# Kernel optimization log

Hardware: AMD Instinct MI355X
Metric: run time of the kernel (lower is better)

The kernel has to match this reference:

```python
import jax, jax.numpy as jnp
import numpy as np
import math

N_EMBD = 768
N_HEAD = 8
HEAD_DIM = N_EMBD // N_HEAD


def new_gelu(x):
    c = math.sqrt(2.0 / math.pi)
    return 0.5 * x * (1.0 + jnp.tanh(c * (x + 0.044715 * x * x * x)))


def layer_norm(x, gamma, beta, eps=1e-5):
    mean = jnp.mean(x, axis=-1, keepdims=True)
    var = jnp.maximum(jnp.mean(x * x, axis=-1, keepdims=True) - mean * mean, 0.0)
    return (x - mean) * jax.lax.rsqrt(var + eps) * gamma + beta


def setup_inputs() -> dict:
    key = jax.random.key(0)
    ks = jax.random.split(key, 10)
    C = N_EMBD
    s = lambda n: 1.0 / math.sqrt(n)
    return {
        "x": jax.random.normal(ks[0], (8, 1024, C), dtype=jnp.float32),
        "ln1_g": jnp.ones((C,), jnp.float32),
        "ln1_b": jnp.zeros((C,), jnp.float32),
        "ln2_g": jnp.ones((C,), jnp.float32),
        "ln2_b": jnp.zeros((C,), jnp.float32),
        "W_attn": jax.random.normal(ks[1], (3 * C, C), jnp.float32) * s(C),
        "b_attn": jnp.zeros((3 * C,), jnp.float32),
        "W_proj": jax.random.normal(ks[2], (C, C), jnp.float32) * s(C),
        "b_proj": jnp.zeros((C,), jnp.float32),
        "W_fc": jax.random.normal(ks[3], (4 * C, C), jnp.float32) * s(C),
        "b_fc": jnp.zeros((4 * C,), jnp.float32),
        "W_fc_proj": jax.random.normal(ks[4], (C, 4 * C), jnp.float32) * s(4 * C),
        "b_fc_proj": jnp.zeros((C,), jnp.float32),
    }


def reference(x, ln1_g, ln1_b, ln2_g, ln2_b, W_attn, b_attn, W_proj, b_proj,
              W_fc, b_fc, W_fc_proj, b_fc_proj):
    B, T, C = x.shape
    # --- attention branch ---
    x1 = layer_norm(x, ln1_g, ln1_b)
    qkv = jnp.einsum('btc,oc->bto', x1, W_attn) + b_attn  # [B,T,3C]
    q, k, v = jnp.split(qkv, 3, axis=-1)
    q = q.reshape(B, T, N_HEAD, HEAD_DIM).transpose(0, 2, 1, 3)  # [B,H,T,D]
    k = k.reshape(B, T, N_HEAD, HEAD_DIM).transpose(0, 2, 1, 3)
    v = v.reshape(B, T, N_HEAD, HEAD_DIM).transpose(0, 2, 1, 3)
    att = jnp.einsum('bhqd,bhkd->bhqk', q, k) * (1.0 / math.sqrt(HEAD_DIM))
    causal = jnp.tril(jnp.ones((T, T), bool))
    att = jnp.where(causal[None, None], att, -jnp.inf)
    att = jax.nn.softmax(att, axis=-1)
    y = jnp.einsum('bhqk,bhkd->bhqd', att, v)
    y = y.transpose(0, 2, 1, 3).reshape(B, T, C)
    y = jnp.einsum('btc,oc->bto', y, W_proj) + b_proj
    x = x + y
    # --- MLP branch ---
    x2 = layer_norm(x, ln2_g, ln2_b)
    h = new_gelu(jnp.einsum('btc,oc->bto', x2, W_fc) + b_fc)
    m = jnp.einsum('bth,oh->bto', h, W_fc_proj) + b_fc_proj
    return x + m
```

## Files before the change

### kernel.cpp

```cpp
#include <hip/hip_runtime.h>
#include <math.h>


#define MROWS 8192
#define CDIM  768
#define TSEQ  1024

typedef _Float16 f16x8 __attribute__((ext_vector_type(8)));
typedef _Float16 f16x4 __attribute__((ext_vector_type(4)));
typedef float f32x4 __attribute__((ext_vector_type(4)));

__device__ __forceinline__ void async_copy16(void* lds, const void* g) {
    __builtin_amdgcn_global_load_lds(
        (const __attribute__((address_space(1))) unsigned int*)g,
        (__attribute__((address_space(3))) unsigned int*)lds, 16, 0, 0);
}

__device__ __forceinline__ int xcd_swizzle(int orig, int nwg) {
    int q = nwg >> 3, r = nwg & 7;
    int xcd = orig & 7, lid = orig >> 3;
    return (xcd < r ? xcd * (q + 1) : r * (q + 1) + (xcd - r) * q) + lid;
}

__device__ __forceinline__ float fast_gelu(float u) {
    float inner = 0.7978845608028654f * (u + 0.044715f * u * u * u);
    float e = __expf(2.0f * inner);
    float th = 1.0f - 2.0f / (e + 1.0f);
    return 0.5f * u * (1.0f + th);
}

__global__ __launch_bounds__(256) void f2h4_kernel(const float* __restrict__ i0,
                                                   const float* __restrict__ i1,
                                                   const float* __restrict__ i2,
                                                   const float* __restrict__ i3,
                                                   _Float16* __restrict__ o0,
                                                   _Float16* __restrict__ o1,
                                                   _Float16* __restrict__ o2,
                                                   _Float16* __restrict__ o3) {
    int bb = blockIdx.x;
    const float* in;
    _Float16* out;
    int lb;
    if (bb < 432)       { in = i0; out = o0; lb = bb; }
    else if (bb < 576)  { in = i1; out = o1; lb = bb - 432; }
    else if (bb < 1152) { in = i2; out = o2; lb = bb - 576; }
    else                { in = i3; out = o3; lb = bb - 1152; }
    int i = lb * 1024 + threadIdx.x;
#pragma unroll
    for (int p = 0; p < 4; ++p, i += 256) {
        float4 v = reinterpret_cast<const float4*>(in)[i];
        f16x4 h;
        h[0] = (_Float16)v.x; h[1] = (_Float16)v.y;
        h[2] = (_Float16)v.z; h[3] = (_Float16)v.w;
        reinterpret_cast<f16x4*>(out)[i] = h;
    }
}

__global__ __launch_bounds__(256) void ln_kernel(const float* __restrict__ x,
                                                 const float* __restrict__ g,
                                                 const float* __restrict__ bta,
                                                 _Float16* __restrict__ out) {
    int row = blockIdx.x;
    int t = threadIdx.x;
    const float* xr = x + (size_t)row * CDIM;
    float v0 = xr[t], v1 = xr[t + 256], v2 = xr[t + 512];
    float s = v0 + v1 + v2;
    float q = v0 * v0 + v1 * v1 + v2 * v2;
#pragma unroll
    for (int o = 32; o; o >>= 1) {
        s += __shfl_xor(s, o);
        q += __shfl_xor(q, o);
    }
    __shared__ float ls[4], lq[4];
    int w = t >> 6, lane = t & 63;
    if (lane == 0) { ls[w] = s; lq[w] = q; }
    __syncthreads();
    s = ls[0] + ls[1] + ls[2] + ls[3];
    q = lq[0] + lq[1] + lq[2] + lq[3];
    float mean = s * (1.0f / CDIM);
    float var = fmaxf(q * (1.0f / CDIM) - mean * mean, 0.0f);
    float rstd = rsqrtf(var + 1e-5f);
    _Float16* orow = out + (size_t)row * CDIM;
    orow[t]       = (_Float16)((v0 - mean) * rstd * g[t]       + bta[t]);
    orow[t + 256] = (_Float16)((v1 - mean) * rstd * g[t + 256] + bta[t + 256]);
    orow[t + 512] = (_Float16)((v2 - mean) * rstd * g[t + 512] + bta[t + 512]);
}

template <int EPI, typename OutT>
__global__ __launch_bounds__(256) void hgemm(const _Float16* __restrict__ A,
                                             const _Float16* __restrict__ W,
                                             const float* __restrict__ bias,
                                             const float* __restrict__ res,
                                             OutT* __restrict__ out,
                                             int M, int N, int K) {
    __shared__ _Float16 As[128 * 32];
    __shared__ _Float16 Bs[128 * 32];
    const int t = threadIdx.x;
    const int wid = t >> 6;
    const int l = t & 63;
    const int fr = l & 15;
    const int fq = l >> 4;
    const int wr = wid >> 1, wc = wid & 1;

    const int nx = gridDim.x;
    const int wg = xcd_swizzle(blockIdx.y * nx + blockIdx.x, nx * gridDim.y);
    const int row0 = (wg / nx) * 128, col0 = (wg % nx) * 128;

    const _Float16* ga = A + (size_t)row0 * K;
    const _Float16* gb = W + (size_t)col0 * K;

    f32x4 acc[4][4] = {};
    const int r_st = t >> 2, c_st = (t & 3) * 8;

    for (int k0 = 0; k0 < K; k0 += 32) {
        __syncthreads();
#pragma unroll
        for (int p = 0; p < 2; ++p) {
            char* la = (char*)As + wid * 1024 + p * 4096;
            char* lb = (char*)Bs + wid * 1024 + p * 4096;
            int r = r_st + p * 64;
            async_copy16(la, ga + (size_t)r * K + k0 + c_st);
            async_copy16(lb, gb + (size_t)r * K + k0 + c_st);
        }
        __syncthreads();

        f16x8 af[4], bf[4];
#pragma unroll
        for (int m = 0; m < 4; ++m)
            af[m] = *reinterpret_cast<const f16x8*>(&As[(wr * 64 + m * 16 + fr) * 32 + fq * 8]);
#pragma unroll
        for (int n = 0; n < 4; ++n)
            bf[n] = *reinterpret_cast<const f16x8*>(&Bs[(wc * 64 + n * 16 + fr) * 32 + fq * 8]);
#pragma unroll
        for (int m = 0; m < 4; ++m)
#pragma unroll
            for (int n = 0; n < 4; ++n)
                acc[m][n] = __builtin_amdgcn_mfma_f32_16x16x32_f16(af[m], bf[n], acc[m][n], 0, 0, 0);
    }

#pragma unroll
    for (int m = 0; m < 4; ++m) {
#pragma unroll
        for (int j = 0; j < 4; ++j) {
            int r = row0 + wr * 64 + m * 16 + fq * 4 + j;
#pragma unroll
            for (int n = 0; n < 4; ++n) {
                int c = col0 + wc * 64 + n * 16 + fr;
                float v = acc[m][n][j] + bias[c];
                if (EPI == 1) v += res[(size_t)r * N + c];
                if (EPI == 2) v = fast_gelu(v);
                out[(size_t)r * N + c] = (OutT)v;
            }
        }
    }
}

template <int EPI, typename OutT>
__global__ __launch_bounds__(256) void hgemm64(const _Float16* __restrict__ A,
                                               const _Float16* __restrict__ W,
                                               const float* __restrict__ bias,
                                               const float* __restrict__ res,
                                               OutT* __restrict__ out,
                                               int M, int N, int K) {
    __shared__ _Float16 As[64 * 32];
    __shared__ _Float16 Bs[128 * 32];
    const int t = threadIdx.x;
    const int wid = t >> 6;
    const int l = t & 63;
    const int fr = l & 15;
    const int fq = l >> 4;
    const int wr = wid >> 1, wc = wid & 1;

    const int nx = gridDim.x;
    const int wg = xcd_swizzle(blockIdx.y * nx + blockIdx.x, nx * gridDim.y);
    const int row0 = (wg / nx) * 64, col0 = (wg % nx) * 128;

    const _Float16* ga = A + (size_t)row0 * K;
    const _Float16* gb = W + (size_t)col0 * K;

    f32x4 acc[2][4] = {};
    const int rl = l >> 2, cl = (l & 3) * 8;

    for (int k0 = 0; k0 < K; k0 += 32) {
        __syncthreads();
        async_copy16((char*)As + wid * 1024, ga + (size_t)(wid * 16 + rl) * K + k0 + cl);
#pragma unroll
        for (int p = 0; p < 2; ++p)
            async_copy16((char*)Bs + wid * 2048 + p * 1024,
                         gb + (size_t)(wid * 32 + p * 16 + rl) * K + k0 + cl);
        __syncthreads();

        f16x8 af[2], bf[4];
#pragma unroll
        for (int m = 0; m < 2; ++m)
            af[m] = *reinterpret_cast<const f16x8*>(&As[(wr * 32 + m * 16 + fr) * 32 + fq * 8]);
#pragma unroll
        for (int n = 0; n < 4; ++n)
            bf[n] = *reinterpret_cast<const f16x8*>(&Bs[(wc * 64 + n * 16 + fr) * 32 + fq * 8]);
#pragma unroll
        for (int m = 0; m < 2; ++m)
#pragma unroll
            for (int n = 0; n < 4; ++n)
                acc[m][n] = __builtin_amdgcn_mfma_f32_16x16x32_f16(af[m], bf[n], acc[m][n], 0, 0, 0);
    }

#pragma unroll
    for (int m = 0; m < 2; ++m) {
#pragma unroll
        for (int j = 0; j < 4; ++j) {
            int r = row0 + wr * 32 + m * 16 + fq * 4 + j;
#pragma unroll
            for (int n = 0; n < 4; ++n) {
                int c = col0 + wc * 64 + n * 16 + fr;
                float v = acc[m][n][j] + bias[c];
                if (EPI == 1) v += res[(size_t)r * N + c];
                if (EPI == 2) v = fast_gelu(v);
                out[(size_t)r * N + c] = (OutT)v;
            }
        }
    }
}

__global__ __launch_bounds__(256) void attn_kernel(const _Float16* __restrict__ qkv,
                                                   _Float16* __restrict__ y) {
    const int bx = blockIdx.x;
    const int bh = blockIdx.y;
    const int b = bh >> 3, h = bh & 7;
    const int t = threadIdx.x;
    const int wid = t >> 6, l = t & 63;
    const int fr = l & 15, fq = l >> 4;

    __shared__ _Float16 Ks[64 * 104];
    __shared__ _Float16 Vt[96 * 72];
    __shared__ _Float16 Ps[64 * 72];

    const size_t base = (size_t)b * TSEQ * 2304 + h * 96;
    const float scale = 0.10206207261596577f;

    const int kkey = t >> 2, kc = t & 3;
    const int vkey = l, vrow = wid;

    for (int ph = 0; ph < 2; ++ph) {
        const int qt = ph ? (15 - bx) : bx;
        const int q0 = qt * 64;
        const int qrow_g = q0 + wid * 16 + fr;

        f16x8 qa[3];
#pragma unroll
        for (int s = 0; s < 3; ++s)
            qa[s] = *reinterpret_cast<const f16x8*>(
                &qkv[base + (size_t)qrow_g * 2304 + s * 32 + fq * 8]);

        f32x4 O[6] = {};
        float m_i[4], l_i[4];
#pragma unroll
        for (int jj = 0; jj < 4; ++jj) { m_i[jj] = -1e30f; l_i[jj] = 0.0f; }

        f16x8 kreg[3], vreg[3];
#pragma unroll
        for (int p = 0; p < 3; ++p) {
            kreg[p] = *reinterpret_cast<const f16x8*>(
                &qkv[base + (size_t)kkey * 2304 + 768 + 8 * (kc + 4 * p)]);
            vreg[p] = *reinterpret_cast<const f16x8*>(
                &qkv[base + (size_t)vkey * 2304 + 1536 + 8 * (vrow + 4 * p)]);
        }

        for (int kt = 0; kt <= qt; ++kt) {
            __syncthreads();
#pragma unroll
            for (int p = 0; p < 3; ++p)
                *reinterpret_cast<f16x8*>(&Ks[kkey * 104 + 8 * (kc + 4 * p)]) = kreg[p];
#pragma unroll
            for (int p = 0; p < 3; ++p) {
                int dr = 8 * (vrow + 4 * p);
#pragma unroll
                for (int e = 0; e < 8; ++e)
                    Vt[(dr + e) * 72 + vkey] = vreg[p][e];
            }
            __syncthreads();

            if (kt < qt) {
                const int k0n = (kt + 1) * 64;
#pragma unroll
                for (int p = 0; p < 3; ++p) {
                    kreg[p] = *reinterpret_cast<const f16x8*>(
                        &qkv[base + (size_t)(k0n + kkey) * 2304 + 768 + 8 * (kc + 4 * p)]);
                    vreg[p] = *reinterpret_cast<const f16x8*>(
                        &qkv[base + (size_t)(k0n + vkey) * 2304 + 1536 + 8 * (vrow + 4 * p)]);
                }
            }

            f32x4 S[4];
#pragma unroll
            for (int n = 0; n < 4; ++n) {
                f32x4 acc = {};
#pragma unroll
                for (int s = 0; s < 3; ++s) {
                    f16x8 kf = *reinterpret_cast<const f16x8*>(
                        &Ks[(n * 16 + fr) * 104 + s * 32 + fq * 8]);
                    acc = __builtin_amdgcn_mfma_f32_16x16x32_f16(qa[s], kf, acc, 0, 0, 0);
                }
                S[n] = acc;
            }

            const bool diag = (kt == qt);
#pragma unroll
            for (int jj = 0; jj < 4; ++jj) {
                float s0 = S[0][jj] * scale, s1 = S[1][jj] * scale;
                float s2 = S[2][jj] * scale, s3 = S[3][jj] * scale;
                if (diag) {
                    int r = wid * 16 + fq * 4 + jj;
                    if (fr > r)      s0 = -1e30f;
                    if (fr + 16 > r) s1 = -1e30f;
                    if (fr + 32 > r) s2 = -1e30f;
                    if (fr + 48 > r) s3 = -1e30f;
                }
                float mx = fmaxf(fmaxf(s0, s1), fmaxf(s2, s3));
#pragma unroll
                for (int off = 8; off; off >>= 1) mx = fmaxf(mx, __shfl_xor(mx, off, 16));
                float mnew = fmaxf(m_i[jj], mx);
                float sf = __expf(m_i[jj] - mnew);
                m_i[jj] = mnew;
                float p0 = __expf(s0 - mnew), p1 = __expf(s1 - mnew);
                float p2 = __expf(s2 - mnew), p3 = __expf(s3 - mnew);
                float rs = p0 + p1 + p2 + p3;
#pragma unroll
                for (int off = 8; off; off >>= 1) rs += __shfl_xor(rs, off, 16);
                l_i[jj] = l_i[jj] * sf + rs;
                const int prow = wid * 16 + fq * 4 + jj;
                Ps[prow * 72 + fr]      = (_Float16)p0;
                Ps[prow * 72 + 16 + fr] = (_Float16)p1;
                Ps[prow * 72 + 32 + fr] = (_Float16)p2;
                Ps[prow * 72 + 48 + fr] = (_Float16)p3;
#pragma unroll
                for (int n = 0; n < 6; ++n) O[n][jj] *= sf;
            }

#pragma unroll
            for (int ks = 0; ks < 2; ++ks) {
                f16x8 pf = *reinterpret_cast<const f16x8*>(
                    &Ps[(wid * 16 + fr) * 72 + ks * 32 + fq * 8]);
#pragma unroll
                for (int n = 0; n < 6; ++n) {
                    f16x8 vf = *reinterpret_cast<const f16x8*>(
                        &Vt[(n * 16 + fr) * 72 + ks * 32 + fq * 8]);
                    O[n] = __builtin_amdgcn_mfma_f32_16x16x32_f16(pf, vf, O[n], 0, 0, 0);
                }
            }
        }

#pragma unroll
        for (int jj = 0; jj < 4; ++jj) {
            const int q = q0 + wid * 16 + fq * 4 + jj;
            const float invl = 1.0f / l_i[jj];
            _Float16* yr = y + ((size_t)b * TSEQ + q) * CDIM + h * 96;
#pragma unroll
            for (int n = 0; n < 6; ++n)
                yr[n * 16 + fr] = (_Float16)(O[n][jj] * invl);
        }
    }
}

extern "C" void kernel_launch(void* const* d_in, const int* in_sizes, int n_in,
                              void* d_out, int out_size, void* d_ws, size_t ws_size,
                              hipStream_t stream) {
    const float* x        = (const float*)d_in[0];
    const float* ln1_g    = (const float*)d_in[1];
    const float* ln1_b    = (const float*)d_in[2];
    const float* ln2_g    = (const float*)d_in[3];
    const float* ln2_b    = (const float*)d_in[4];
    const float* W_attn   = (const float*)d_in[5];
    const float* b_attn   = (const float*)d_in[6];
    const float* W_proj   = (const float*)d_in[7];
    const float* b_proj   = (const float*)d_in[8];
    const float* W_fc     = (const float*)d_in[9];
    const float* b_fc     = (const float*)d_in[10];
    const float* W_fcproj = (const float*)d_in[11];
    const float* b_fcproj = (const float*)d_in[12];
    float* out = (float*)d_out;

    _Float16* qkvh  = (_Float16*)d_ws;
    _Float16* actsh = qkvh + (size_t)MROWS * 2304;
    _Float16* hh    = actsh + (size_t)MROWS * CDIM;
    _Float16* wah   = hh + (size_t)MROWS * 3072;
    _Float16* wph   = wah + (size_t)2304 * 768;
    _Float16* wfh   = wph + (size_t)768 * 768;
    _Float16* wfph  = wfh + (size_t)3072 * 768;

    dim3 blk(256);

    f2h4_kernel<<<dim3(1728), blk, 0, stream>>>(W_attn, W_proj, W_fc, W_fcproj,
                                                wah, wph, wfh, wfph);

    ln_kernel<<<dim3(MROWS), blk, 0, stream>>>(x, ln1_g, ln1_b, actsh);
    hgemm<0, _Float16><<<dim3(2304 / 128, MROWS / 128), blk, 0, stream>>>(
        actsh, wah, b_attn, nullptr, qkvh, MROWS, 2304, CDIM);
    attn_kernel<<<dim3(8, 64), blk, 0, stream>>>(qkvh, actsh);
    hgemm64<1, float><<<dim3(CDIM / 128, MROWS / 64), blk, 0, stream>>>(
        actsh, wph, b_proj, x, out, MROWS, CDIM, CDIM);
    ln_kernel<<<dim3(MROWS), blk, 0, stream>>>(out, ln2_g, ln2_b, actsh);
    hgemm<2, _Float16><<<dim3(3072 / 128, MROWS / 128), blk, 0, stream>>>(
        actsh, wfh, b_fc, nullptr, hh, MROWS, 3072, CDIM);
    hgemm64<1, float><<<dim3(CDIM / 128, MROWS / 64), blk, 0, stream>>>(
        hh, wfph, b_fcproj, out, out, MROWS, CDIM, 3072);
}
```

Measured before the change: 406.2 us.

## Double-buffer LDS tiles in GEMM kernels to overlap global loads with MFMA

Both GEMM kernels now use two LDS buffers per operand and issue the async global-to-LDS copy for the next K tile before computing on the current one. This replaces the two barriers per K step with one, so memory latency can hide behind the MFMA work. It doubles LDS use per block, which may lower occupancy. The loop is unrolled by two and assumes an even tile count; K values of 768 and 3072 give even counts. The barrier at the end of each step relies on the compiler inserting a wait for the outstanding copies before it, which could race if it does not.

```diff
diff --git a/kernel.cpp b/kernel.cpp
--- a/kernel.cpp
+++ b/kernel.cpp
@@ -93,8 +93,8 @@
                                              const float* __restrict__ res,
                                              OutT* __restrict__ out,
                                              int M, int N, int K) {
-    __shared__ _Float16 As[128 * 32];
-    __shared__ _Float16 Bs[128 * 32];
+    __shared__ _Float16 As[2][128 * 32];
+    __shared__ _Float16 Bs[2][128 * 32];
     const int t = threadIdx.x;
     const int wid = t >> 6;
     const int l = t & 63;
@@ -111,31 +111,41 @@
 
     f32x4 acc[4][4] = {};
     const int r_st = t >> 2, c_st = (t & 3) * 8;
-
-    for (int k0 = 0; k0 < K; k0 += 32) {
-        __syncthreads();
+    const int nt = K >> 5;
+
+    auto stage = [&](int buf, int k0) {
 #pragma unroll
         for (int p = 0; p < 2; ++p) {
-            char* la = (char*)As + wid * 1024 + p * 4096;
-            char* lb = (char*)Bs + wid * 1024 + p * 4096;
+            char* la = (char*)&As[buf][0] + wid * 1024 + p * 4096;
+            char* lb = (char*)&Bs[buf][0] + wid * 1024 + p * 4096;
             int r = r_st + p * 64;
             async_copy16(la, ga + (size_t)r * K + k0 + c_st);
             async_copy16(lb, gb + (size_t)r * K + k0 + c_st);
         }
-        __syncthreads();
-
+    };
+
+    auto step = [&](int buf, int tt) {
+        if (tt + 1 < nt) stage(buf ^ 1, (tt + 1) << 5);
         f16x8 af[4], bf[4];
 #pragma unroll
         for (int m = 0; m < 4; ++m)
-            af[m] = *reinterpret_cast<const f16x8*>(&As[(wr * 64 + m * 16 + fr) * 32 + fq * 8]);
+            af[m] = *reinterpret_cast<const f16x8*>(&As[buf][(wr * 64 + m * 16 + fr) * 32 + fq * 8]);
 #pragma unroll
         for (int n = 0; n < 4; ++n)
-            bf[n] = *reinterpret_cast<const f16x8*>(&Bs[(wc * 64 + n * 16 + fr) * 32 + fq * 8]);
+            bf[n] = *reinterpret_cast<const f16x8*>(&Bs[buf][(wc * 64 + n * 16 + fr) * 32 + fq * 8]);
 #pragma unroll
         for (int m = 0; m < 4; ++m)
 #pragma unroll
             for (int n = 0; n < 4; ++n)
                 acc[m][n] = __builtin_amdgcn_mfma_f32_16x16x32_f16(af[m], bf[n], acc[m][n], 0, 0, 0);
+        __syncthreads();
+    };
+
+    stage(0, 0);
+    __syncthreads();
+    for (int tt = 0; tt < nt; tt += 2) {
+        step(0, tt);
+        step(1, tt + 1);
     }
 
 #pragma unroll
@@ -162,8 +172,8 @@
                                                const float* __restrict__ res,
                                                OutT* __restrict__ out,
                                                int M, int N, int K) {
-    __shared__ _Float16 As[64 * 32];
-    __shared__ _Float16 Bs[128 * 32];
+    __shared__ _Float16 As[2][64 * 32];
+    __shared__ _Float16 Bs[2][128 * 32];
     const int t = threadIdx.x;
     const int wid = t >> 6;
     const int l = t & 63;
@@ -180,28 +190,39 @@
 
     f32x4 acc[2][4] = {};
     const int rl = l >> 2, cl = (l & 3) * 8;
-
-    for (int k0 = 0; k0 < K; k0 += 32) {
-        __syncthreads();
-        async_copy16((char*)As + wid * 1024, ga + (size_t)(wid * 16 + rl) * K + k0 + cl);
+    const int nt = K >> 5;
+
+    auto stage = [&](int buf, int k0) {
+        async_copy16((char*)&As[buf][0] + wid * 1024,
+                     ga + (size_t)(wid * 16 + rl) * K + k0 + cl);
 #pragma unroll
         for (int p = 0; p < 2; ++p)
-            async_copy16((char*)Bs + wid * 2048 + p * 1024,
+            async_copy16((char*)&Bs[buf][0] + wid * 2048 + p * 1024,
                          gb + (size_t)(wid * 32 + p * 16 + rl) * K + k0 + cl);
-        __syncthreads();
-
+    };
+
+    auto step = [&](int buf, int tt) {
+        if (tt + 1 < nt) stage(buf ^ 1, (tt + 1) << 5);
         f16x8 af[2], bf[4];
 #pragma unroll
         for (int m = 0; m < 2; ++m)
-            af[m] = *reinterpret_cast<const f16x8*>(&As[(wr * 32 + m * 16 + fr) * 32 + fq * 8]);
+            af[m] = *reinterpret_cast<const f16x8*>(&As[buf][(wr * 32 + m * 16 + fr) * 32 + fq * 8]);
 #pragma unroll
         for (int n = 0; n < 4; ++n)
-            bf[n] = *reinterpret_cast<const f16x8*>(&Bs[(wc * 64 + n * 16 + fr) * 32 + fq * 8]);
+            bf[n] = *reinterpret_cast<const f16x8*>(&Bs[buf][(wc * 64 + n * 16 + fr) * 32 + fq * 8]);
 #pragma unroll
         for (int m = 0; m < 2; ++m)
 #pragma unroll
             for (int n = 0; n < 4; ++n)
                 acc[m][n] = __builtin_amdgcn_mfma_f32_16x16x32_f16(af[m], bf[n], acc[m][n], 0, 0, 0);
+        __syncthreads();
+    };
+
+    stage(0, 0);
+    __syncthreads();
+    for (int tt = 0; tt < nt; tt += 2) {
+        step(0, tt);
+        step(1, tt + 1);
     }
 
 #pragma unroll
```

Result: faster. 385.7 us (-5.0%).
